# Kernel tuning notes

Hardware: AMD Instinct MI355X
Metric: run time of the kernel (lower is better)

The kernel has to match this reference:

```python
import jax, jax.numpy as jnp
import numpy as np

B, T, I = 4, 4096, 1024
HEADS, DIM = 16, 64


def _combine(a, b):
    # Log-sum-exp stable combine of running softmax-attention triples.
    # a, b: tuples (m, u, w) with m,u: (B,T,H), w: (B,T,H,D)
    ma, ua, wa = a
    mb, ub, wb = b
    m = jnp.maximum(ma, mb)
    ea = jnp.exp(ma - m)
    eb = jnp.exp(mb - m)
    u = ua * ea + ub * eb
    w = wa * ea[..., None] + wb * eb[..., None]
    return (m, u, w)


def setup_inputs() -> dict:
    key = jax.random.key(0)
    k1, k2, k3 = jax.random.split(key, 3)
    inputs = jax.random.normal(k1, (B, T, I), dtype=jnp.float32)
    # glorot-ish scale for kernels
    kv_kernel = jax.random.normal(k2, (I, HEADS, DIM, 2), dtype=jnp.float32) * (1.0 / np.sqrt(I))
    q_kernel = jax.random.normal(k3, (HEADS, DIM), dtype=jnp.float32) * (1.0 / np.sqrt(DIM))
    return {"inputs": inputs, "kv_kernel": kv_kernel, "q_kernel": q_kernel, "training": 0}


def reference(inputs, kv_kernel, q_kernel, training):
    # kv projection: (B,T,I) x (I,H,D,2) -> (B,T,H,D,2)
    kv = jnp.einsum('bti,ihdk->bthdk', inputs, kv_kernel)
    kv = jax.nn.silu(kv)  # activation='silu'; dropout is identity at inference
    k = kv[..., 0]  # (B,T,H,D)
    v = kv[..., 1]  # (B,T,H,D)
    # per-head learned query: scores (B,T,H)
    s = jnp.einsum('hd,bthd->bth', q_kernel, k)
    # initial triples per timestep: (m=s, u=1, w=v)
    m0 = s
    u0 = jnp.ones_like(s)
    w0 = v
    m, u, w = jax.lax.associative_scan(_combine, (m0, u0, w0), axis=1)
    # prefix softmax attention output: numerator / denominator -> (B,T,H,D)
    return w / u[..., None]
```

## Files before the change

### kernel.cpp

```cpp
#include <hip/hip_runtime.h>
#include <hip/hip_bf16.h>
#include <stdint.h>

#define B_ 4
#define T_ 4096
#define I_ 1024
#define H_ 16
#define D_ 64
#define M_TOT (B_*T_)
#define N_TOT (H_*D_*2)
#define K_TOT I_

#define BM 256
#define BN 128
#define BK 64
#define NT (K_TOT/BK)
#define BUF_ELEMS (BM*BK + BN*BK)

typedef __bf16 bf16;
typedef __attribute__((ext_vector_type(8))) __bf16 bf16x8;
typedef __attribute__((ext_vector_type(4))) float f32x4;

#define AS_G __attribute__((address_space(1)))
#define AS_L __attribute__((address_space(3)))

__device__ __forceinline__ void gld_lds16(const void* g, void* l) {
    __builtin_amdgcn_global_load_lds((const AS_G void*)g, (AS_L void*)l, 16, 0, 0);
}

__global__ void k_prep(const float* __restrict__ x, const float* __restrict__ w,
                       bf16* __restrict__ xb, bf16* __restrict__ wt) {
    if (blockIdx.x < 2048) {
        int idx = blockIdx.x * 256 + threadIdx.x;
        const int n4 = (M_TOT * K_TOT) / 4;
        for (int i = idx; i < n4; i += 2048 * 256) {
            float4 f = reinterpret_cast<const float4*>(x)[i];
            union { bf16 h[4]; uint64_t u; } pk;
            pk.h[0] = (bf16)f.x; pk.h[1] = (bf16)f.y; pk.h[2] = (bf16)f.z; pk.h[3] = (bf16)f.w;
            reinterpret_cast<uint64_t*>(xb)[i] = pk.u;
        }
    } else {
        __shared__ float tile[32][33];
        int bid = blockIdx.x - 2048;
        int tn = bid % (N_TOT/32);
        int ti = bid / (N_TOT/32);
        int tid = threadIdx.x;
        int c = tid & 31, rgrp = tid >> 5;
        #pragma unroll
        for (int p = 0; p < 4; ++p) {
            int il = p * 8 + rgrp;
            int cn = tn*32 + c;
            int h = cn >> 7, k2 = (cn >> 6) & 1, d = cn & 63;
            int nsrc = (h << 7) + (d << 1) + k2;
            tile[il][c] = w[(ti*32 + il) * N_TOT + nsrc];
        }
        __syncthreads();
        #pragma unroll
        for (int p = 0; p < 4; ++p) {
            int nl = p * 8 + rgrp;
            wt[(size_t)(tn*32 + nl) * K_TOT + ti*32 + c] = (bf16)tile[c][nl];
        }
    }
}

__device__ __forceinline__ bf16x8 frag(const bf16* base, int row, int slot) {
    const char* p = (const char*)base + row * 128 + (((slot ^ (row & 7)) & 7) << 4);
    return *reinterpret_cast<const bf16x8*>(p);
}

__global__ __launch_bounds__(512, 2)
void k_gemm(const bf16* __restrict__ xb, const bf16* __restrict__ wt,
            const float* __restrict__ q, bf16* __restrict__ v, float* __restrict__ s) {
    extern __shared__ __attribute__((aligned(16))) char smem[];
    bf16* lds = (bf16*)smem;

    const int tid = threadIdx.x;
    const int wid = tid >> 6, lane = tid & 63;
    const int wm = wid >> 1, wn = wid & 1;
    const int g = lane >> 4, r16 = lane & 15;

    int bid = blockIdx.x;
    int swz = (bid & 7) * 128 + (bid >> 3);
    int bm = swz >> 4, bn = swz & 15;
    const int row0 = bm * BM;
    const int n0 = bn * BN;
    const int h = bn;

    auto stageA = [&](int bi, int t) {
        bf16* dst = lds + bi * BUF_ELEMS;
        int k0 = t * BK;
        #pragma unroll
        for (int j = 0; j < 4; ++j) {
            int c = j * 512 + tid;
            int row = c >> 3, p = c & 7;
            gld_lds16(xb + (size_t)(row0 + row) * K_TOT + k0 + ((p ^ (row & 7)) << 3), dst + c * 8);
        }
    };
    auto stageB = [&](int bi, int t) {
        bf16* dst = lds + bi * BUF_ELEMS + BM * BK;
        int k0 = t * BK;
        #pragma unroll
        for (int j = 0; j < 2; ++j) {
            int c = j * 512 + tid;
            int row = c >> 3, p = c & 7;
            gld_lds16(wt + (size_t)(n0 + row) * K_TOT + k0 + ((p ^ (row & 7)) << 3), dst + c * 8);
        }
    };

    f32x4 acc[4][4];
    #pragma unroll
    for (int i = 0; i < 4; ++i)
        #pragma unroll
        for (int j = 0; j < 4; ++j) acc[i][j] = (f32x4){0.f,0.f,0.f,0.f};

    stageA(0, 0); stageB(0, 0);
    stageA(1, 1); stageB(1, 1);
    asm volatile("s_waitcnt vmcnt(6)" ::: "memory");
    __builtin_amdgcn_s_barrier();

    #pragma unroll 1
    for (int t = 0; t < NT; ++t) {
        const int cur = t % 3;
        const int nx2 = (t + 2) % 3;
        const bf16* Ab = lds + cur * BUF_ELEMS;
        const bf16* Bb = Ab + BM * BK;
        const bool st = (t + 2 < NT);
        bf16x8 a[4], b[4];

        #pragma unroll
        for (int mi = 0; mi < 4; ++mi) a[mi] = frag(Ab, wm*64 + mi*16 + r16, g);
        #pragma unroll
        for (int ni = 0; ni < 4; ++ni) b[ni] = frag(Bb, wn*64 + ni*16 + r16, g);
        if (st) stageA(nx2, t + 2);
        __builtin_amdgcn_s_barrier();
        __builtin_amdgcn_s_setprio(1);
        #pragma unroll
        for (int mi = 0; mi < 4; ++mi)
            #pragma unroll
            for (int ni = 0; ni < 4; ++ni)
                acc[mi][ni] = __builtin_amdgcn_mfma_f32_16x16x32_bf16(a[mi], b[ni], acc[mi][ni], 0,0,0);
        __builtin_amdgcn_s_setprio(0);
        __builtin_amdgcn_s_barrier();

        #pragma unroll
        for (int mi = 0; mi < 4; ++mi) a[mi] = frag(Ab, wm*64 + mi*16 + r16, 4 + g);
        #pragma unroll
        for (int ni = 0; ni < 4; ++ni) b[ni] = frag(Bb, wn*64 + ni*16 + r16, 4 + g);
        if (st) stageB(nx2, t + 2);
        __builtin_amdgcn_s_barrier();
        __builtin_amdgcn_s_setprio(1);
        #pragma unroll
        for (int mi = 0; mi < 4; ++mi)
            #pragma unroll
            for (int ni = 0; ni < 4; ++ni)
                acc[mi][ni] = __builtin_amdgcn_mfma_f32_16x16x32_bf16(a[mi], b[ni], acc[mi][ni], 0,0,0);
        __builtin_amdgcn_s_setprio(0);
        if (t + 1 < NT) {
            if (st) asm volatile("s_waitcnt vmcnt(6)" ::: "memory");
            else    asm volatile("s_waitcnt vmcnt(0)" ::: "memory");
            __builtin_amdgcn_s_barrier();
        }
    }

    if (wn == 0) {
        float qv[4];
        #pragma unroll
        for (int ni = 0; ni < 4; ++ni) qv[ni] = q[h * D_ + ni*16 + r16];
        #pragma unroll
        for (int mi = 0; mi < 4; ++mi) {
            #pragma unroll
            for (int r = 0; r < 4; ++r) {
                float part = 0.f;
                #pragma unroll
                for (int ni = 0; ni < 4; ++ni) {
                    float x = acc[mi][ni][r];
                    part += (x / (1.0f + __expf(-x))) * qv[ni];
                }
                part += __shfl_xor(part, 1);
                part += __shfl_xor(part, 2);
                part += __shfl_xor(part, 4);
                part += __shfl_xor(part, 8);
                if (r16 == 0) {
                    int row = row0 + wm*64 + mi*16 + g*4 + r;
                    s[row * H_ + h] = part;
                }
            }
        }
    } else {
        #pragma unroll
        for (int mi = 0; mi < 4; ++mi)
            #pragma unroll
            for (int ni = 0; ni < 4; ++ni)
                #pragma unroll
                for (int r = 0; r < 4; ++r) {
                    int row = row0 + wm*64 + mi*16 + g*4 + r;
                    int d = ni*16 + r16;
                    float x = acc[mi][ni][r];
                    v[(size_t)row * (H_*D_) + h*D_ + d] = (bf16)(x / (1.0f + __expf(-x)));
                }
    }
}

__global__ void k_scanA(const float* __restrict__ s, const bf16* __restrict__ v, float* __restrict__ agg) {
    int C = blockIdx.x * 4 + (threadIdx.x >> 6);
    int lane = threadIdx.x & 63;
    int p = C >> 6, c = C & 63;
    int b = p >> 4, h = p & 15;
    int rbase = b * T_ + c * 64;
    const bf16* vbase = v + h * D_ + lane;
    float m = -INFINITY, u = 0.f, w = 0.f;
    #pragma unroll 4
    for (int i = 0; i < 64; ++i) {
        int r = rbase + i;
        float sv = s[r * H_ + h];
        float vv = (float)vbase[(size_t)r * (H_*D_)];
        float mn = fmaxf(m, sv);
        float ea = __expf(m - mn);
        float eb = __expf(sv - mn);
        u = u * ea + eb;
        w = w * ea + vv * eb;
        m = mn;
    }
    float* a = agg + C * 66;
    if (lane == 0) { a[0] = m; a[1] = u; }
    a[2 + lane] = w;
}

__global__ void k_scanB(const float* __restrict__ agg, float* __restrict__ pre) {
    int p = blockIdx.x;
    int lane = threadIdx.x;
    float wreg[64];
    #pragma unroll
    for (int c = 0; c < 64; ++c) wreg[c] = agg[(size_t)(p*64 + c)*66 + 2 + lane];
    float ml = agg[(size_t)(p*64 + lane)*66];
    float ul = agg[(size_t)(p*64 + lane)*66 + 1];
    float m = -INFINITY, u = 0.f, w = 0.f;
    #pragma unroll
    for (int c = 0; c < 64; ++c) {
        float* o = pre + (size_t)(p*64 + c)*66;
        if (lane == 0) { o[0] = m; o[1] = u; }
        o[2 + lane] = w;
        float ma = __shfl(ml, c), ua = __shfl(ul, c), wa = wreg[c];
        float mn = fmaxf(m, ma);
        float ec = __expf(m - mn), ea = __expf(ma - mn);
        u = u * ec + ua * ea;
        w = w * ec + wa * ea;
        m = mn;
    }
}

__global__ void k_scanC(const float* __restrict__ s, const bf16* __restrict__ v,
                        const float* __restrict__ pre, float* __restrict__ out) {
    int C = blockIdx.x * 4 + (threadIdx.x >> 6);
    int lane = threadIdx.x & 63;
    int p = C >> 6, c = C & 63;
    int b = p >> 4, h = p & 15;
    int rbase = b * T_ + c * 64;
    const bf16* vbase = v + h * D_ + lane;
    const float* pr = pre + C * 66;
    float m = pr[0], u = pr[1], w = pr[2 + lane];
    #pragma unroll 4
    for (int i = 0; i < 64; ++i) {
        int r = rbase + i;
        float sv = s[r * H_ + h];
        float vv = (float)vbase[(size_t)r * (H_*D_)];
        float mn = fmaxf(m, sv);
        float ea = __expf(m - mn);
        float eb = __expf(sv - mn);
        u = u * ea + eb;
        w = w * ea + vv * eb;
        m = mn;
        out[(size_t)r * (H_*D_) + h * D_ + lane] = __fdividef(w, u);
    }
}

extern "C" void kernel_launch(void* const* d_in, const int* in_sizes, int n_in,
                              void* d_out, int out_size, void* d_ws, size_t ws_size,
                              hipStream_t stream) {
    (void)in_sizes; (void)n_in; (void)out_size; (void)ws_size;
    const float* x  = (const float*)d_in[0];
    const float* wk = (const float*)d_in[1];
    const float* qk = (const float*)d_in[2];
    float* out = (float*)d_out;
    char* ws = (char*)d_ws;

    bf16*  xb  = (bf16*) (ws);
    bf16*  wt  = (bf16*) (ws + 33554432ull);
    bf16*  v   = (bf16*) (ws + 37748736ull);
    float* s   = (float*)(ws + 71303168ull);
    float* agg = (float*)(ws + 72351744ull);
    float* pre = (float*)(ws + 73433088ull);

    hipLaunchKernelGGL(k_prep,  dim3(4096), dim3(256), 0, stream, x, wk, xb, wt);
    hipLaunchKernelGGL(k_gemm,  dim3((M_TOT/BM)*(N_TOT/BN)), dim3(512), 3*BUF_ELEMS*2, stream, xb, wt, qk, v, s);
    hipLaunchKernelGGL(k_scanA, dim3(B_*H_*64/4), dim3(256), 0, stream, s, v, agg);
    hipLaunchKernelGGL(k_scanB, dim3(B_*H_), dim3(64), 0, stream, agg, pre);
    hipLaunchKernelGGL(k_scanC, dim3(B_*H_*64/4), dim3(256), 0, stream, s, v, pre, out);
}
```

Measured before the change: 243.3 us.

## Fuse chunk-aggregate scan into GEMM epilogue and retile GEMM to 256x256x32

The GEMM tile grows to 256x256 with BK=32 and a 4-stage LDS ring, so each block covers two heads, and SiLU is applied once to all accumulators. The first scan pass (per-64-row chunk m/u/w aggregates) is computed in the GEMM epilogue from registers plus the scores kept in LDS, and the separate k_scanA kernel is removed. This saves a launch and the re-read of v and s. The cost is a larger accumulator footprint (128 floats per thread) at 2 blocks/CU, which risks register pressure or spills, plus a heavier epilogue.

```diff
diff --git a/kernel.cpp b/kernel.cpp
--- a/kernel.cpp
+++ b/kernel.cpp
@@ -12,10 +12,10 @@
 #define K_TOT I_
 
 #define BM 256
-#define BN 128
-#define BK 64
+#define BN 256
+#define BK 32
 #define NT (K_TOT/BK)
-#define BUF_ELEMS (BM*BK + BN*BK)
+#define BUFE (BM*BK + BN*BK)
 
 typedef __bf16 bf16;
 typedef __attribute__((ext_vector_type(8))) __bf16 bf16x8;
@@ -63,75 +63,76 @@
     }
 }
 
-__device__ __forceinline__ bf16x8 frag(const bf16* base, int row, int slot) {
-    const char* p = (const char*)base + row * 128 + (((slot ^ (row & 7)) & 7) << 4);
+__device__ __forceinline__ bf16x8 frag(const bf16* base, int row, int g) {
+    const char* p = (const char*)base + row * 64 + (((g ^ ((row >> 1) & 3)) & 3) << 4);
     return *reinterpret_cast<const bf16x8*>(p);
 }
 
 __global__ __launch_bounds__(512, 2)
 void k_gemm(const bf16* __restrict__ xb, const bf16* __restrict__ wt,
-            const float* __restrict__ q, bf16* __restrict__ v, float* __restrict__ s) {
+            const float* __restrict__ q, bf16* __restrict__ v,
+            float* __restrict__ s, float* __restrict__ agg) {
     extern __shared__ __attribute__((aligned(16))) char smem[];
     bf16* lds = (bf16*)smem;
+    float* s_lds = (float*)(smem + 4*BUFE*2);
 
     const int tid = threadIdx.x;
     const int wid = tid >> 6, lane = tid & 63;
-    const int wm = wid >> 1, wn = wid & 1;
+    const int wm = wid >> 2, wn = wid & 3;
     const int g = lane >> 4, r16 = lane & 15;
 
     int bid = blockIdx.x;
-    int swz = (bid & 7) * 128 + (bid >> 3);
-    int bm = swz >> 4, bn = swz & 15;
-    const int row0 = bm * BM;
-    const int n0 = bn * BN;
-    const int h = bn;
-
-    auto stageA = [&](int bi, int t) {
-        bf16* dst = lds + bi * BUF_ELEMS;
-        int k0 = t * BK;
-        #pragma unroll
-        for (int j = 0; j < 4; ++j) {
-            int c = j * 512 + tid;
-            int row = c >> 3, p = c & 7;
-            gld_lds16(xb + (size_t)(row0 + row) * K_TOT + k0 + ((p ^ (row & 7)) << 3), dst + c * 8);
-        }
-    };
-    auto stageB = [&](int bi, int t) {
-        bf16* dst = lds + bi * BUF_ELEMS + BM * BK;
+    int swz = (bid & 7) * 64 + (bid >> 3);
+    int bm = swz >> 3, bn = swz & 7;
+    const int row0 = bm * BM, n0 = bn * BN;
+
+    auto stageA = [&](int t) {
+        bf16* dst = lds + (t & 3) * BUFE;
         int k0 = t * BK;
         #pragma unroll
         for (int j = 0; j < 2; ++j) {
             int c = j * 512 + tid;
-            int row = c >> 3, p = c & 7;
-            gld_lds16(wt + (size_t)(n0 + row) * K_TOT + k0 + ((p ^ (row & 7)) << 3), dst + c * 8);
+            int row = c >> 2, sl = c & 3;
+            int koff = ((sl ^ ((row >> 1) & 3)) & 3) << 3;
+            gld_lds16(xb + (size_t)(row0 + row) * K_TOT + k0 + koff, (char*)dst + c * 16);
         }
     };
-
-    f32x4 acc[4][4];
+    auto stageB = [&](int t) {
+        bf16* dst = lds + (t & 3) * BUFE + BM * BK;
+        int k0 = t * BK;
+        #pragma unroll
+        for (int j = 0; j < 2; ++j) {
+            int c = j * 512 + tid;
+            int row = c >> 2, sl = c & 3;
+            int koff = ((sl ^ ((row >> 1) & 3)) & 3) << 3;
+            gld_lds16(wt + (size_t)(n0 + row) * K_TOT + k0 + koff, (char*)dst + c * 16);
+        }
+    };
+
+    f32x4 acc[8][4];
     #pragma unroll
-    for (int i = 0; i < 4; ++i)
+    for (int i = 0; i < 8; ++i)
         #pragma unroll
         for (int j = 0; j < 4; ++j) acc[i][j] = (f32x4){0.f,0.f,0.f,0.f};
 
-    stageA(0, 0); stageB(0, 0);
-    stageA(1, 1); stageB(1, 1);
-    asm volatile("s_waitcnt vmcnt(6)" ::: "memory");
+    stageA(0); stageB(0);
+    stageA(1); stageB(1);
+    stageA(2); stageB(2);
+    asm volatile("s_waitcnt vmcnt(8)" ::: "memory");
     __builtin_amdgcn_s_barrier();
 
     #pragma unroll 1
     for (int t = 0; t < NT; ++t) {
-        const int cur = t % 3;
-        const int nx2 = (t + 2) % 3;
-        const bf16* Ab = lds + cur * BUF_ELEMS;
+        const bf16* Ab = lds + (t & 3) * BUFE;
         const bf16* Bb = Ab + BM * BK;
-        const bool st = (t + 2 < NT);
+        const bool st = (t + 3 < NT);
         bf16x8 a[4], b[4];
 
         #pragma unroll
-        for (int mi = 0; mi < 4; ++mi) a[mi] = frag(Ab, wm*64 + mi*16 + r16, g);
+        for (int mi = 0; mi < 4; ++mi) a[mi] = frag(Ab, wm*128 + mi*16 + r16, g);
         #pragma unroll
         for (int ni = 0; ni < 4; ++ni) b[ni] = frag(Bb, wn*64 + ni*16 + r16, g);
-        if (st) stageA(nx2, t + 2);
+        if (st) stageA(t + 3);
         __builtin_amdgcn_s_barrier();
         __builtin_amdgcn_s_setprio(1);
         #pragma unroll
@@ -143,87 +144,118 @@
         __builtin_amdgcn_s_barrier();
 
         #pragma unroll
-        for (int mi = 0; mi < 4; ++mi) a[mi] = frag(Ab, wm*64 + mi*16 + r16, 4 + g);
-        #pragma unroll
-        for (int ni = 0; ni < 4; ++ni) b[ni] = frag(Bb, wn*64 + ni*16 + r16, 4 + g);
-        if (st) stageB(nx2, t + 2);
+        for (int mi = 0; mi < 4; ++mi) a[mi] = frag(Ab, wm*128 + (mi+4)*16 + r16, g);
+        if (st) stageB(t + 3);
         __builtin_amdgcn_s_barrier();
         __builtin_amdgcn_s_setprio(1);
         #pragma unroll
         for (int mi = 0; mi < 4; ++mi)
             #pragma unroll
             for (int ni = 0; ni < 4; ++ni)
-                acc[mi][ni] = __builtin_amdgcn_mfma_f32_16x16x32_bf16(a[mi], b[ni], acc[mi][ni], 0,0,0);
+                acc[mi+4][ni] = __builtin_amdgcn_mfma_f32_16x16x32_bf16(a[mi], b[ni], acc[mi+4][ni], 0,0,0);
         __builtin_amdgcn_s_setprio(0);
-        if (t + 1 < NT) {
-            if (st) asm volatile("s_waitcnt vmcnt(6)" ::: "memory");
-            else    asm volatile("s_waitcnt vmcnt(0)" ::: "memory");
+        if (t < NT - 1) {
+            if (t < NT - 3)       asm volatile("s_waitcnt vmcnt(8)" ::: "memory");
+            else if (t == NT - 3) asm volatile("s_waitcnt vmcnt(4)" ::: "memory");
+            else                  asm volatile("s_waitcnt vmcnt(0)" ::: "memory");
             __builtin_amdgcn_s_barrier();
         }
     }
 
-    if (wn == 0) {
+    #pragma unroll
+    for (int mi = 0; mi < 8; ++mi)
+        #pragma unroll
+        for (int ni = 0; ni < 4; ++ni)
+            #pragma unroll
+            for (int r = 0; r < 4; ++r) {
+                float x = acc[mi][ni][r];
+                acc[mi][ni][r] = x / (1.0f + __expf(-x));
+            }
+
+    const int hloc = wn >> 1;
+    const int h = bn * 2 + hloc;
+
+    if ((wn & 1) == 0) {
         float qv[4];
         #pragma unroll
         for (int ni = 0; ni < 4; ++ni) qv[ni] = q[h * D_ + ni*16 + r16];
         #pragma unroll
-        for (int mi = 0; mi < 4; ++mi) {
+        for (int mi = 0; mi < 8; ++mi) {
             #pragma unroll
             for (int r = 0; r < 4; ++r) {
-                float part = 0.f;
-                #pragma unroll
-                for (int ni = 0; ni < 4; ++ni) {
-                    float x = acc[mi][ni][r];
-                    part += (x / (1.0f + __expf(-x))) * qv[ni];
-                }
+                float part = acc[mi][0][r]*qv[0] + acc[mi][1][r]*qv[1]
+                           + acc[mi][2][r]*qv[2] + acc[mi][3][r]*qv[3];
                 part += __shfl_xor(part, 1);
                 part += __shfl_xor(part, 2);
                 part += __shfl_xor(part, 4);
                 part += __shfl_xor(part, 8);
                 if (r16 == 0) {
-                    int row = row0 + wm*64 + mi*16 + g*4 + r;
-                    s[row * H_ + h] = part;
+                    int rl = wm*128 + mi*16 + g*4 + r;
+                    s[(row0 + rl) * H_ + h] = part;
+                    s_lds[hloc*256 + rl] = part;
                 }
             }
         }
     } else {
         #pragma unroll
-        for (int mi = 0; mi < 4; ++mi)
+        for (int mi = 0; mi < 8; ++mi)
             #pragma unroll
             for (int ni = 0; ni < 4; ++ni)
                 #pragma unroll
                 for (int r = 0; r < 4; ++r) {
-                    int row = row0 + wm*64 + mi*16 + g*4 + r;
-                    int d = ni*16 + r16;
-                    float x = acc[mi][ni][r];
-                    v[(size_t)row * (H_*D_) + h*D_ + d] = (bf16)(x / (1.0f + __expf(-x)));
+                    int row = row0 + wm*128 + mi*16 + g*4 + r;
+                    v[(size_t)row * (H_*D_) + h*D_ + ni*16 + r16] = (bf16)acc[mi][ni][r];
                 }
     }
-}
-
-__global__ void k_scanA(const float* __restrict__ s, const bf16* __restrict__ v, float* __restrict__ agg) {
-    int C = blockIdx.x * 4 + (threadIdx.x >> 6);
-    int lane = threadIdx.x & 63;
-    int p = C >> 6, c = C & 63;
-    int b = p >> 4, h = p & 15;
-    int rbase = b * T_ + c * 64;
-    const bf16* vbase = v + h * D_ + lane;
-    float m = -INFINITY, u = 0.f, w = 0.f;
-    #pragma unroll 4
-    for (int i = 0; i < 64; ++i) {
-        int r = rbase + i;
-        float sv = s[r * H_ + h];
-        float vv = (float)vbase[(size_t)r * (H_*D_)];
-        float mn = fmaxf(m, sv);
-        float ea = __expf(m - mn);
-        float eb = __expf(sv - mn);
-        u = u * ea + eb;
-        w = w * ea + vv * eb;
-        m = mn;
-    }
-    float* a = agg + C * 66;
-    if (lane == 0) { a[0] = m; a[1] = u; }
-    a[2 + lane] = w;
+    __syncthreads();
+
+    if (wn & 1) {
+        #pragma unroll
+        for (int c = 0; c < 2; ++c) {
+            float sv[16];
+            #pragma unroll
+            for (int mm = 0; mm < 4; ++mm)
+                #pragma unroll
+                for (int r = 0; r < 4; ++r)
+                    sv[mm*4+r] = s_lds[hloc*256 + wm*128 + (c*4+mm)*16 + g*4 + r];
+            float m_l = sv[0];
+            #pragma unroll
+            for (int i = 1; i < 16; ++i) m_l = fmaxf(m_l, sv[i]);
+            float u_l = 0.f, w_l[4] = {0.f, 0.f, 0.f, 0.f};
+            #pragma unroll
+            for (int mm = 0; mm < 4; ++mm)
+                #pragma unroll
+                for (int r = 0; r < 4; ++r) {
+                    float e = __expf(sv[mm*4+r] - m_l);
+                    u_l += e;
+                    #pragma unroll
+                    for (int ni = 0; ni < 4; ++ni)
+                        w_l[ni] += e * acc[c*4+mm][ni][r];
+                }
+            #pragma unroll
+            for (int off = 16; off <= 32; off <<= 1) {
+                float m2 = __shfl_xor(m_l, off);
+                float u2 = __shfl_xor(u_l, off);
+                float w2[4];
+                #pragma unroll
+                for (int ni = 0; ni < 4; ++ni) w2[ni] = __shfl_xor(w_l[ni], off);
+                float mn = fmaxf(m_l, m2);
+                float ea = __expf(m_l - mn), eb = __expf(m2 - mn);
+                u_l = u_l * ea + u2 * eb;
+                #pragma unroll
+                for (int ni = 0; ni < 4; ++ni) w_l[ni] = w_l[ni]*ea + w2[ni]*eb;
+                m_l = mn;
+            }
+            if (g == 0) {
+                int rbase = row0 + wm*128 + c*64;
+                int bb = rbase >> 12, tloc = rbase & (T_-1);
+                float* a = agg + (size_t)(((bb*H_ + h) << 6) + (tloc >> 6)) * 66;
+                if (r16 == 0) { a[0] = m_l; a[1] = u_l; }
+                #pragma unroll
+                for (int ni = 0; ni < 4; ++ni) a[2 + ni*16 + r16] = w_l[ni];
+            }
+        }
+    }
 }
 
 __global__ void k_scanB(const float* __restrict__ agg, float* __restrict__ pre) {
@@ -292,8 +324,8 @@
     float* pre = (float*)(ws + 73433088ull);
 
     hipLaunchKernelGGL(k_prep,  dim3(4096), dim3(256), 0, stream, x, wk, xb, wt);
-    hipLaunchKernelGGL(k_gemm,  dim3((M_TOT/BM)*(N_TOT/BN)), dim3(512), 3*BUF_ELEMS*2, stream, xb, wt, qk, v, s);
-    hipLaunchKernelGGL(k_scanA, dim3(B_*H_*64/4), dim3(256), 0, stream, s, v, agg);
+    hipLaunchKernelGGL(k_gemm,  dim3((M_TOT/BM)*(N_TOT/BN)), dim3(512), 4*BUFE*2 + 2048, stream,
+                       xb, wt, qk, v, s, agg);
     hipLaunchKernelGGL(k_scanB, dim3(B_*H_), dim3(64), 0, stream, agg, pre);
     hipLaunchKernelGGL(k_scanC, dim3(B_*H_*64/4), dim3(256), 0, stream, s, v, pre, out);
 }
```

Result: faster. 232.9 us (-4.2%).
